# Performance work log

Measured on AMD Instinct MI355X. Metric: run time of the kernel, lower is better.

## Reference

```python
import jax, jax.numpy as jnp
import numpy as np

B, QL, DL = 256, 16, 512      # batch, query len, doc graph nodes
ND, NW, ED = 512, 50000, 300  # n_docs, vocab, embed dim
TOPK, K2, K4 = 40, 240, 192   # args.topk, ggnn2 keep, ggnn4 keep


def setup_inputs() -> dict:
    key = jax.random.key(0)
    ks = jax.random.split(key, 32)
    s = 0.1
    inp = {
        "emb": jax.random.normal(ks[0], (NW + 1, ED), jnp.float32),
        "qrl_token": jax.random.randint(ks[1], (B, QL), 0, NW),
        "doc_token": jax.random.randint(ks[2], (B, DL), 0, NW),
        "doc_ids": jax.random.randint(ks[3], (B,), 0, ND),
        "docs_adj": jax.random.uniform(ks[4], (ND, DL, DL), jnp.float32),
        "idf": jax.random.uniform(ks[5], (B, QL, 1), jnp.float32),
        "W_g1": jax.random.normal(ks[6], (6, QL, QL), jnp.float32) * s,
        "b_g1": jax.random.normal(ks[7], (6, QL), jnp.float32) * s,
        "w_g2": jax.random.normal(ks[8], (6,), jnp.float32) * s,
        "b_g2": jax.random.normal(ks[9], (6,), jnp.float32) * s,
        "W_g3": jax.random.normal(ks[10], (6, QL, QL), jnp.float32) * s,
        "b_g3": jax.random.normal(ks[11], (6, QL), jnp.float32) * s,
        "w_g4": jax.random.normal(ks[12], (6,), jnp.float32) * s,
        "b_g4": jax.random.normal(ks[13], (6,), jnp.float32) * s,
        "p1_w": jax.random.normal(ks[14], (QL,), jnp.float32) * s,
        "p1_b": jax.random.normal(ks[15], (1,), jnp.float32) * s,
        "p2_w": jax.random.normal(ks[16], (QL,), jnp.float32) * s,
        "p2_b": jax.random.normal(ks[17], (1,), jnp.float32) * s,
        "l1_w": jax.random.normal(ks[18], (64, 3 * TOPK), jnp.float32) * s,
        "l1_b": jax.random.normal(ks[19], (64,), jnp.float32) * s,
        "l2_w": jax.random.normal(ks[20], (32, 64), jnp.float32) * s,
        "l2_b": jax.random.normal(ks[21], (32,), jnp.float32) * s,
        "l3_w": jax.random.normal(ks[22], (1, 32), jnp.float32) * s,
        "l3_b": jax.random.normal(ks[23], (1,), jnp.float32) * s,
        "gated_w": jax.random.normal(ks[24], (1,), jnp.float32) * s,
        "gated_b": jax.random.normal(ks[25], (1,), jnp.float32) * s,
    }
    return inp


def _simmat(a_emb, b_emb):
    # cosine similarity [B, A, C]
    an = jnp.linalg.norm(a_emb, axis=2)[:, :, None] + 1e-9
    bn = jnp.linalg.norm(b_emb, axis=2)[:, None, :] + 1e-9
    return jnp.einsum("bad,bcd->bac", a_emb, b_emb) / (an * bn)


def _gate_mat(a, x, W, b):
    # GGNN gated update, W: [6, D, D] stacked (z0,z1,r0,r1,h0,h1)
    lin = lambda t, i: t @ W[i].T + b[i]
    z = jax.nn.sigmoid(lin(a, 0) + lin(x, 1))
    r = jax.nn.sigmoid(lin(a, 2) + lin(x, 3))
    h = jax.nn.relu(lin(a, 4) + lin(r * x, 5))
    return h * z + x * (1.0 - z)


def _gate_scalar(a, x, w, b):
    lin = lambda t, i: t * w[i] + b[i]
    z = jax.nn.sigmoid(lin(a, 0) + lin(x, 1))
    r = jax.nn.sigmoid(lin(a, 2) + lin(x, 3))
    h = jax.nn.relu(lin(a, 4) + lin(r * x, 5))
    return h * z + x * (1.0 - z)


def _sub_adj(A, idx):
    # A: [L, L], idx: [K] -> A[idx][:, idx]
    return A[idx][:, idx]


def reference(emb, qrl_token, doc_token, doc_ids, docs_adj, idf,
              W_g1, b_g1, w_g2, b_g2, W_g3, b_g3, w_g4, b_g4,
              p1_w, p1_b, p2_w, p2_b,
              l1_w, l1_b, l2_w, l2_b, l3_w, l3_b, gated_w, gated_b):
    qe = emb[qrl_token]               # [B, QL, ED]
    de = emb[doc_token]               # [B, DL, ED]
    feat = _simmat(qe, de).transpose(0, 2, 1)   # [B, DL, QL]
    topk0 = jax.lax.top_k(feat.transpose(0, 2, 1), TOPK)[0]  # [B, QL, TOPK]

    adj = docs_adj[doc_ids]           # [B, DL, DL]

    # ggnn1
    rep1 = _gate_mat(adj @ feat, feat, W_g1, b_g1)           # [B, DL, QL]

    # ggnn2 (scalar gates on projected feature + topk subgraph gather)
    x2 = rep1 @ p1_w[:, None] + p1_b                         # [B, DL, 1]
    feat_s = _gate_scalar(adj @ x2, x2, w_g2, b_g2)          # [B, DL, 1]
    score1, idx1 = jax.lax.top_k(feat_s[..., 0], K2)         # [B, K2]
    att_x1 = jnp.take_along_axis(rep1, idx1[:, :, None], axis=1)  # [B, K2, QL]
    adj_new = jax.vmap(_sub_adj)(adj, idx1)                  # [B, K2, K2]
    att_x1 = jnp.tanh(score1)[:, :, None] * att_x1

    # ggnn3
    rep3 = _gate_mat(adj_new @ att_x1, att_x1, W_g3, b_g3)   # [B, K2, QL]

    # ggnn4
    x4 = rep3 @ p2_w[:, None] + p2_b                         # [B, K2, 1]
    feat_s4 = _gate_scalar(adj_new @ x4, x4, w_g4, b_g4)
    score2, idx2 = jax.lax.top_k(feat_s4[..., 0], K4)        # [B, K4]
    att_x2 = jnp.take_along_axis(rep3, idx2[:, :, None], axis=1)  # [B, K4, QL]
    att_x2 = jnp.tanh(score2)[:, :, None] * att_x2

    att1 = jax.lax.top_k(att_x1.transpose(0, 2, 1), TOPK)[0]  # [B, QL, TOPK]
    att2 = jax.lax.top_k(att_x2.transpose(0, 2, 1), TOPK)[0]  # [B, QL, TOPK]
    att_x = jnp.concatenate([topk0, att1, att2], axis=-1)     # [B, QL, 3*TOPK]

    rel = jax.nn.relu(att_x @ l1_w.T + l1_b)
    rel = jax.nn.relu(rel @ l2_w.T + l2_b)
    rel = rel @ l3_w.T + l3_b                                 # [B, QL, 1]

    gated_weight = jax.nn.softmax(idf * gated_w + gated_b, axis=1)
    rel = rel * gated_weight
    scores = rel[..., 0].sum(-1, keepdims=True)               # [B, 1]
    return scores
```

## Files before the change

### kernel.cpp

```cpp
#include <hip/hip_runtime.h>
#include <math.h>

#define B_   256
#define QL_  16
#define DL_  512
#define ED_  300
#define K2_  240
#define K4_  192
#define NEGINF (-3.402823466e38f)

__device__ __forceinline__ float sigf(float x){ return 1.0f/(1.0f+__expf(-x)); }

__device__ __forceinline__ float dot16(const float (&a)[16], const float* w){
  float s = 0.f;
  #pragma unroll
  for (int i=0;i<4;i++){
    float4 ww = *(const float4*)(w + 4*i);
    s = fmaf(a[4*i+0], ww.x, s);
    s = fmaf(a[4*i+1], ww.y, s);
    s = fmaf(a[4*i+2], ww.z, s);
    s = fmaf(a[4*i+3], ww.w, s);
  }
  return s;
}

template<int N, int T>
__device__ void bitonic_desc(float* v, int* id){
  const int tid = threadIdx.x;
  for (int k = 2; k <= N; k <<= 1){
    for (int j = k >> 1; j > 0; j >>= 1){
      __syncthreads();
      for (int i = tid; i < N; i += T){
        const int l = i ^ j;
        if (l > i){
          const float vi = v[i], vl = v[l];
          const int ii = id[i], il = id[l];
          const bool before_l = (vl > vi) || (vl == vi && il < ii);
          const bool up = ((i & k) == 0);
          if (up == before_l){ v[i]=vl; v[l]=vi; id[i]=il; id[l]=ii; }
        }
      }
    }
  }
  __syncthreads();
}

template<int NREG>
__device__ __forceinline__ void wave_sort_desc(float (&v)[NREG], int lane){
  constexpr int TOT = NREG*64;
  #pragma unroll
  for (int k = 2; k <= TOT; k <<= 1){
    #pragma unroll
    for (int j = k>>1; j > 0; j >>= 1){
      if (j >= 64){
        const int jr = j >> 6;
        #pragma unroll
        for (int r = 0; r < NREG; r++){
          if ((r & jr) == 0){
            const int p = r | jr;
            const bool desc = (((r*64) & k) == 0);
            const float a = v[r], c = v[p];
            const float mx = fmaxf(a,c), mn = fminf(a,c);
            v[r] = desc ? mx : mn;
            v[p] = desc ? mn : mx;
          }
        }
      } else {
        #pragma unroll
        for (int r = 0; r < NREG; r++){
          const float ov = __shfl_xor(v[r], j);
          const bool desc = (((r*64 + lane) & k) == 0);
          const bool lower = (lane & j) == 0;
          v[r] = (lower == desc) ? fmaxf(v[r], ov) : fminf(v[r], ov);
        }
      }
    }
  }
}

__global__ __launch_bounds__(256) void k_feat(
    const float* __restrict__ emb, const int* __restrict__ qtok,
    const int* __restrict__ dtok,
    float* __restrict__ featdq, float* __restrict__ featqd)
{
  alignas(16) __shared__ float ql[16*304];
  __shared__ float qinv[16];
  __shared__ int toks[128];
  const int tid = threadIdx.x;
  const int b = blockIdx.x >> 2, d0 = (blockIdx.x & 3) * 128;
  #pragma unroll
  for (int q=0;q<16;q++){
    const int tokq = qtok[(size_t)b*QL_ + q];
    for (int e=tid; e<ED_; e+=256)
      ql[q*304+e] = emb[(size_t)tokq*ED_ + e];
  }
  if (tid < 128) toks[tid] = dtok[(size_t)b*DL_ + d0 + tid];
  __syncthreads();
  {
    const int q = tid >> 4, s = tid & 15;
    float ss = 0.f;
    for (int e=s;e<ED_;e+=16){ const float x = ql[q*304+e]; ss = fmaf(x,x,ss); }
    ss += __shfl_xor(ss,1); ss += __shfl_xor(ss,2);
    ss += __shfl_xor(ss,4); ss += __shfl_xor(ss,8);
    if (s == 0) qinv[q] = 1.f/(sqrtf(ss)+1e-9f);
  }
  __syncthreads();
  const int g = tid>>2, sub = tid&3;
  const float* e0p = emb + (size_t)toks[2*g+0]*ED_;
  const float* e1p = emb + (size_t)toks[2*g+1]*ED_;
  float acc[2][16];
  float ssr[2] = {0.f,0.f};
  #pragma unroll
  for (int r=0;r<2;r++)
    #pragma unroll
    for (int q=0;q<16;q++) acc[r][q] = 0.f;
  for (int i=0;i<19;i++){
    const int j = sub + 4*i;
    if (j < 75){
      const int e0 = 4*j;
      float4 d0v = *(const float4*)(e0p + e0);
      float4 d1v = *(const float4*)(e1p + e0);
      ssr[0] = fmaf(d0v.x,d0v.x, fmaf(d0v.y,d0v.y, fmaf(d0v.z,d0v.z, fmaf(d0v.w,d0v.w, ssr[0]))));
      ssr[1] = fmaf(d1v.x,d1v.x, fmaf(d1v.y,d1v.y, fmaf(d1v.z,d1v.z, fmaf(d1v.w,d1v.w, ssr[1]))));
      #pragma unroll
      for (int q=0;q<16;q++){
        float4 qv = *(const float4*)(&ql[q*304 + e0]);
        acc[0][q] = fmaf(d0v.x,qv.x, fmaf(d0v.y,qv.y, fmaf(d0v.z,qv.z, fmaf(d0v.w,qv.w, acc[0][q]))));
        acc[1][q] = fmaf(d1v.x,qv.x, fmaf(d1v.y,qv.y, fmaf(d1v.z,qv.z, fmaf(d1v.w,qv.w, acc[1][q]))));
      }
    }
  }
  #pragma unroll
  for (int r=0;r<2;r++){
    #pragma unroll
    for (int q=0;q<16;q++){
      float v = acc[r][q];
      v += __shfl_xor(v, 1);
      v += __shfl_xor(v, 2);
      acc[r][q] = v;
    }
    float sv = ssr[r];
    sv += __shfl_xor(sv, 1);
    sv += __shfl_xor(sv, 2);
    ssr[r] = sv;
  }
  const int r = sub & 1;
  const int d = d0 + 2*g + r;
  const float ssd = r ? ssr[1] : ssr[0];
  const float invd = 1.f/(sqrtf(ssd)+1e-9f);
  float vs[16];
  #pragma unroll
  for (int q=0;q<16;q++){
    const float v = r ? acc[1][q] : acc[0][q];
    vs[q] = v * invd * qinv[q];
  }
  if (sub < 2){
    float* fo = &featdq[((size_t)b*DL_ + d)*16];
    *(float4*)(fo+0)  = make_float4(vs[0],vs[1],vs[2],vs[3]);
    *(float4*)(fo+4)  = make_float4(vs[4],vs[5],vs[6],vs[7]);
    *(float4*)(fo+8)  = make_float4(vs[8],vs[9],vs[10],vs[11]);
    *(float4*)(fo+12) = make_float4(vs[12],vs[13],vs[14],vs[15]);
  } else {
    #pragma unroll
    for (int q=0;q<16;q++)
      featqd[((size_t)b*QL_+q)*DL_ + d] = vs[q];
  }
}

__global__ __launch_bounds__(256,3) void k_gemm512(
    const float* __restrict__ dadj, const int* __restrict__ doc_ids,
    const float* __restrict__ Bmat, const float* __restrict__ Wg,
    const float* __restrict__ bg, const float* __restrict__ pw,
    const float* __restrict__ pb, float* __restrict__ rep,
    float* __restrict__ xproj)
{
  __shared__ float fx[512*20];
  __shared__ float wl[1536];
  __shared__ float bl[96];
  __shared__ float pwl[16];
  const int tid = threadIdx.x;
  const int b = blockIdx.x >> 1, part = blockIdx.x & 1;
  const int m0 = part * 256;
  for (int idx = tid; idx < 512*16; idx += 256){
    fx[(idx>>4)*20 + (idx&15)] = Bmat[(size_t)b*512*16 + idx];
  }
  for (int idx = tid; idx < 1536; idx += 256) wl[idx] = Wg[idx];
  if (tid < 96) bl[tid] = bg[tid];
  if (tid < 16) pwl[tid] = pw[tid];
  __syncthreads();

  const int g = tid >> 2, sub = tid & 3;
  const int mb = m0 + 4*g;
  {
    const int lda = 512;
    const float* arow = dadj + (size_t)doc_ids[b] * 512 * 512;
    const float* r0 = arow + (size_t)mb * lda;
    constexpr int ITERS = 32;
    float acc[4][16];
    #pragma unroll
    for (int r=0;r<4;r++)
      #pragma unroll
      for (int q=0;q<16;q++) acc[r][q] = 0.f;
    int kk = sub*4;
    float4 c0 = *(const float4*)(r0 + kk);
    float4 c1 = *(const float4*)(r0 + lda + kk);
    float4 c2 = *(const float4*)(r0 + 2*lda + kk);
    float4 c3 = *(const float4*)(r0 + 3*lda + kk);
    for (int i = 0; i < ITERS; i++){
      const int kn = kk + ((i < ITERS-1) ? 16 : 0);
      float4 n0 = *(const float4*)(r0 + kn);
      float4 n1 = *(const float4*)(r0 + lda + kn);
      float4 n2 = *(const float4*)(r0 + 2*lda + kn);
      float4 n3 = *(const float4*)(r0 + 3*lda + kn);
      const float av[4][4] = {{c0.x,c0.y,c0.z,c0.w},{c1.x,c1.y,c1.z,c1.w},
                              {c2.x,c2.y,c2.z,c2.w},{c3.x,c3.y,c3.z,c3.w}};
      #pragma unroll
      for (int c = 0; c < 4; c++){
        const float* fr = &fx[(size_t)(kk + c)*20];
        float4 q0 = *(const float4*)(fr);
        float4 q1 = *(const float4*)(fr+4);
        float4 q2 = *(const float4*)(fr+8);
        float4 q3 = *(const float4*)(fr+12);
        const float qv[16] = {q0.x,q0.y,q0.z,q0.w, q1.x,q1.y,q1.z,q1.w,
                              q2.x,q2.y,q2.z,q2.w, q3.x,q3.y,q3.z,q3.w};
        #pragma unroll
        for (int r = 0; r < 4; r++){
          const float a_ = av[r][c];
          #pragma unroll
          for (int q = 0; q < 16; q++)
            acc[r][q] = fmaf(a_, qv[q], acc[r][q]);
        }
      }
      c0 = n0; c1 = n1; c2 = n2; c3 = n3;
      kk += 16;
    }
    #pragma unroll
    for (int r=0;r<4;r++)
      #pragma unroll
      for (int q=0;q<16;q++){
        float v = acc[r][q];
        v += __shfl_xor(v, 1);
        v += __shfl_xor(v, 2);
        acc[r][q] = v;
      }
    const int m = mb + sub;
    float a[16], x[16];
    #pragma unroll
    for (int q=0;q<16;q++)
      a[q] = (sub==0)?acc[0][q]:(sub==1)?acc[1][q]:(sub==2)?acc[2][q]:acc[3][q];
    {
      const float* xr = &fx[(size_t)m*20];
      float4 x0 = *(const float4*)(xr),   x1 = *(const float4*)(xr+4);
      float4 x2v = *(const float4*)(xr+8), x3 = *(const float4*)(xr+12);
      x[0]=x0.x; x[1]=x0.y; x[2]=x0.z; x[3]=x0.w;
      x[4]=x1.x; x[5]=x1.y; x[6]=x1.z; x[7]=x1.w;
      x[8]=x2v.x; x[9]=x2v.y; x[10]=x2v.z; x[11]=x2v.w;
      x[12]=x3.x; x[13]=x3.y; x[14]=x3.z; x[15]=x3.w;
    }
    float z[16], rr[16];
    #pragma unroll
    for (int q=0;q<16;q++){
      const float s0 = bl[q] + bl[16+q]
                     + dot16(a, &wl[q*16]) + dot16(x, &wl[256 + q*16]);
      z[q] = sigf(s0);
      const float s1 = bl[32+q] + bl[48+q]
                     + dot16(a, &wl[512 + q*16]) + dot16(x, &wl[768 + q*16]);
      rr[q] = sigf(s1);
    }
    float rx[16];
    #pragma unroll
    for (int q=0;q<16;q++) rx[q] = rr[q]*x[q];
    float out[16]; float xp = 0.f;
    #pragma unroll
    for (int q=0;q<16;q++){
      const float s = bl[64+q] + bl[80+q]
                    + dot16(a, &wl[1024 + q*16]) + dot16(rx, &wl[1280 + q*16]);
      const float h = fmaxf(s, 0.f);
      const float o = h*z[q] + x[q]*(1.f - z[q]);
      out[q] = o;
      xp = fmaf(o, pwl[q], xp);
    }
    float* rp = &rep[((size_t)b*512 + m)*16];
    *(float4*)(rp+0)  = make_float4(out[0],out[1],out[2],out[3]);
    *(float4*)(rp+4)  = make_float4(out[4],out[5],out[6],out[7]);
    *(float4*)(rp+8)  = make_float4(out[8],out[9],out[10],out[11]);
    *(float4*)(rp+12) = make_float4(out[12],out[13],out[14],out[15]);
    xproj[(size_t)b*512 + m] = xp + pb[0];
  }
}

__global__ __launch_bounds__(1024) void k_chain(
    const float* __restrict__ dadj, const int* __restrict__ dids,
    const float* __restrict__ featqd, const float* __restrict__ rep1,
    const float* __restrict__ x2g,
    const float* __restrict__ wg2, const float* __restrict__ bg2,
    const float* __restrict__ Wg3, const float* __restrict__ bg3,
    const float* __restrict__ wg4, const float* __restrict__ bg4,
    const float* __restrict__ p2w, const float* __restrict__ p2b,
    const float* __restrict__ l1w, const float* __restrict__ l1b,
    const float* __restrict__ l2w, const float* __restrict__ l2b,
    const float* __restrict__ l3w, const float* __restrict__ l3b,
    const float* __restrict__ idf, const float* __restrict__ gw,
    const float* __restrict__ gb,
    float* __restrict__ adjnew, float* __restrict__ outp)
{
  extern __shared__ float sm[];
  float* fx   = sm;
  float* repl = fx + 4800;
  float* w1l  = repl + 4800;
  float* w2l  = w1l + 7936;
  float* wl   = w2l + 2176;
  float* attl = wl + 1536;
  float* rel1 = attl + 1920;
  float* rel2 = rel1 + 1024;
  float* xv   = rel2 + 512;
  float* sval = xv + 512;
  int*   sidx = (int*)(sval + 512);
  int*   il   = sidx + 512;
  float* bl   = (float*)(il + 240);
  float* pwl  = bl + 96;

  const int tid = threadIdx.x, b = blockIdx.x;
  const int wave = tid >> 6, lane = tid & 63;
  const float* abase = dadj + (size_t)dids[b]*512*512;

  if (tid < 512) xv[tid] = x2g[(size_t)b*512 + tid];
  __syncthreads();

  if (wave < 8){
    const int g = tid >> 2, sub = tid & 3;
    const float w0=wg2[0],w1=wg2[1],w2=wg2[2],w3=wg2[3],w4=wg2[4],w5=wg2[5];
    const float c0=bg2[0],c1=bg2[1],c2=bg2[2],c3=bg2[3],c4=bg2[4],c5=bg2[5];
    for (int p = 0; p < 4; p++){
      const int m = p*128 + g;
      const float* row = abase + (size_t)m*512;
      float s = 0.f;
      #pragma unroll 4
      for (int i=0;i<32;i++){
        const int kk = i*16 + sub*4;
        float4 a4 = *(const float4*)(row + kk);
        float4 xq = *(const float4*)(&xv[kk]);
        s = fmaf(a4.x,xq.x,s); s = fmaf(a4.y,xq.y,s);
        s = fmaf(a4.z,xq.z,s); s = fmaf(a4.w,xq.w,s);
      }
      s += __shfl_xor(s,1); s += __shfl_xor(s,2);
      if (sub == 0){
        const float x = xv[m];
        const float z = sigf(fmaf(s,w0,c0) + fmaf(x,w1,c1));
        const float r = sigf(fmaf(s,w2,c2) + fmaf(x,w3,c3));
        const float h = fmaxf(fmaf(s,w4,c4) + fmaf(r*x,w5,c5), 0.f);
        sval[m] = h*z + x*(1.f - z);
        sidx[m] = m;
      }
    }
  } else {
    const int w8 = wave - 8;
    #pragma unroll
    for (int t=0;t<2;t++){
      const int q = w8*2 + t;
      const float* src = featqd + ((size_t)b*QL_ + q)*512;
      float v[8];
      #pragma unroll
      for (int r=0;r<8;r++) v[r] = src[lane + 64*r];
      wave_sort_desc<8>(v, lane);
      if (lane < 40) attl[q*120 + lane] = v[0];
    }
    for (int idx = tid-512; idx < 7680; idx += 512){
      const int u = idx/120, k2 = idx - u*120;
      w1l[u*124 + k2] = l1w[idx];
    }
    for (int idx = tid-512; idx < 2048; idx += 512)
      w2l[(idx>>6)*68 + (idx&63)] = l2w[idx];
  }
  bitonic_desc<512,1024>(sval, sidx);

  if (tid < K2_){
    const int rowi = sidx[tid];
    il[tid] = rowi;
    const float tv = tanhf(sval[tid]);
    const float* rr = rep1 + ((size_t)b*512 + rowi)*16;
    float4 r0 = *(const float4*)(rr),   r1 = *(const float4*)(rr+4);
    float4 r2 = *(const float4*)(rr+8), r3 = *(const float4*)(rr+12);
    float* o = &fx[(size_t)tid*20];
    *(float4*)(o+0)  = make_float4(tv*r0.x,tv*r0.y,tv*r0.z,tv*r0.w);
    *(float4*)(o+4)  = make_float4(tv*r1.x,tv*r1.y,tv*r1.z,tv*r1.w);
    *(float4*)(o+8)  = make_float4(tv*r2.x,tv*r2.y,tv*r2.z,tv*r2.w);
    *(float4*)(o+12) = make_float4(tv*r3.x,tv*r3.y,tv*r3.z,tv*r3.w);
  }
  __syncthreads();

  for (int idx = tid; idx < 1536; idx += 1024) wl[idx] = Wg3[idx];
  if (tid < 96) bl[tid] = bg3[tid];
  if (tid < 16) pwl[tid] = p2w[tid];
  {
    const int rt = wave, jt = lane;
    int jc[4];
    #pragma unroll
    for (int c=0;c<4;c++){
      const int j = jt + 64*c;
      jc[c] = (j < K2_) ? il[j] : 0;
    }
    for (int p=0;p<15;p++){
      const int r = rt + p*16;
      const float* row = abase + (size_t)il[r]*512;
      float* orow = adjnew + ((size_t)b*K2_ + r)*K2_;
      #pragma unroll
      for (int c=0;c<4;c++){
        const int j = jt + 64*c;
        if (j < K2_) orow[j] = row[jc[c]];
      }
    }
  }
  __syncthreads();

  {
    const int q = wave;
    float v[4];
    #pragma unroll
    for (int r=0;r<4;r++){
      const int idx = lane + 64*r;
      v[r] = (idx < K2_) ? fx[(size_t)idx*20 + q] : NEGINF;
    }
    wave_sort_desc<4>(v, lane);
    if (lane < 40) attl[q*120 + 40 + lane] = v[0];
  }

  {
    const int g = tid >> 2, sub = tid & 3;
    if (g < K2_){
      const int m = g;
      const float* r0 = adjnew + ((size_t)b*K2_ + m)*K2_;
      float acc[16];
      #pragma unroll
      for (int q=0;q<16;q++) acc[q] = 0.f;
      for (int i=0;i<15;i++){
        const int kk = i*16 + sub*4;
        float4 a4 = *(const float4*)(r0 + kk);
        const float av[4] = {a4.x, a4.y, a4.z, a4.w};
        #pragma unroll
        for (int c=0;c<4;c++){
          const float* fr = &fx[(size_t)(kk + c)*20];
          float4 q0 = *(const float4*)(fr);
          float4 q1 = *(const float4*)(fr+4);
          float4 q2 = *(const float4*)(fr+8);
          float4 q3 = *(const float4*)(fr+12);
          const float qv[16] = {q0.x,q0.y,q0.z,q0.w, q1.x,q1.y,q1.z,q1.w,
                                q2.x,q2.y,q2.z,q2.w, q3.x,q3.y,q3.z,q3.w};
          #pragma unroll
          for (int q=0;q<16;q++)
            acc[q] = fmaf(av[c], qv[q], acc[q]);
        }
      }
      #pragma unroll
      for (int q=0;q<16;q++){
        float v = acc[q];
        v += __shfl_xor(v, 1);
        v += __shfl_xor(v, 2);
        acc[q] = v;
      }
      float x[16];
      {
        const float* xr = &fx[(size_t)m*20];
        float4 x0 = *(const float4*)(xr),   x1 = *(const float4*)(xr+4);
        float4 x2v = *(const float4*)(xr+8), x3 = *(const float4*)(xr+12);
        x[0]=x0.x; x[1]=x0.y; x[2]=x0.z; x[3]=x0.w;
        x[4]=x1.x; x[5]=x1.y; x[6]=x1.z; x[7]=x1.w;
        x[8]=x2v.x; x[9]=x2v.y; x[10]=x2v.z; x[11]=x2v.w;
        x[12]=x3.x; x[13]=x3.y; x[14]=x3.z; x[15]=x3.w;
      }
      float rx[16];
      #pragma unroll
      for (int q=0;q<16;q++){
        const float s1 = bl[32+q] + bl[48+q]
                       + dot16(acc, &wl[512 + q*16]) + dot16(x, &wl[768 + q*16]);
        rx[q] = sigf(s1) * x[q];
      }
      float xp = 0.f;
      #pragma unroll
      for (int j=0;j<4;j++){
        const int q = sub*4 + j;
        const float s0 = bl[q] + bl[16+q]
                       + dot16(acc, &wl[q*16]) + dot16(x, &wl[256 + q*16]);
        const float z = sigf(s0);
        const float s = bl[64+q] + bl[80+q]
                      + dot16(acc, &wl[1024 + q*16]) + dot16(rx, &wl[1280 + q*16]);
        const float h = fmaxf(s, 0.f);
        const float o = h*z + x[q]*(1.f - z);
        repl[(size_t)m*20 + q] = o;
        xp = fmaf(o, pwl[q], xp);
      }
      xp += __shfl_xor(xp,1); xp += __shfl_xor(xp,2);
      if (sub == 0) xv[m] = xp + p2b[0];
    }
  }
  __syncthreads();

  {
    const int g = tid >> 2, sub = tid & 3;
    const float w0=wg4[0],w1=wg4[1],w2=wg4[2],w3=wg4[3],w4=wg4[4],w5=wg4[5];
    const float c0=bg4[0],c1=bg4[1],c2=bg4[2],c3=bg4[3],c4=bg4[4],c5=bg4[5];
    if (g < K2_){
      const float* row = adjnew + ((size_t)b*K2_ + g)*K2_;
      float s = 0.f;
      #pragma unroll
      for (int i=0;i<15;i++){
        const int kk = i*16 + sub*4;
        float4 a4 = *(const float4*)(row + kk);
        float4 xq = *(const float4*)(&xv[kk]);
        s = fmaf(a4.x,xq.x,s); s = fmaf(a4.y,xq.y,s);
        s = fmaf(a4.z,xq.z,s); s = fmaf(a4.w,xq.w,s);
      }
      s += __shfl_xor(s,1); s += __shfl_xor(s,2);
      if (sub == 0){
        const float x = xv[g];
        const float z = sigf(fmaf(s,w0,c0) + fmaf(x,w1,c1));
        const float r = sigf(fmaf(s,w2,c2) + fmaf(x,w3,c3));
        const float h = fmaxf(fmaf(s,w4,c4) + fmaf(r*x,w5,c5), 0.f);
        sval[g] = h*z + x*(1.f - z);
        sidx[g] = g;
      }
    }
    if (tid >= 960 && tid < 976){
      sval[K2_ + tid - 960] = NEGINF;
      sidx[K2_ + tid - 960] = 0x7fffffff;
    }
  }
  bitonic_desc<256,1024>(sval, sidx);

  if (tid < K4_){
    const int rowi = sidx[tid];
    const float tv = tanhf(sval[tid]);
    const float* rr = &repl[(size_t)rowi*20];
    float4 r0 = *(const float4*)(rr),   r1 = *(const float4*)(rr+4);
    float4 r2 = *(const float4*)(rr+8), r3 = *(const float4*)(rr+12);
    float* o = &fx[(size_t)tid*20];
    *(float4*)(o+0)  = make_float4(tv*r0.x,tv*r0.y,tv*r0.z,tv*r0.w);
    *(float4*)(o+4)  = make_float4(tv*r1.x,tv*r1.y,tv*r1.z,tv*r1.w);
    *(float4*)(o+8)  = make_float4(tv*r2.x,tv*r2.y,tv*r2.z,tv*r2.w);
    *(float4*)(o+12) = make_float4(tv*r3.x,tv*r3.y,tv*r3.z,tv*r3.w);
  }
  __syncthreads();

  {
    const int q = wave;
    float v[4];
    #pragma unroll
    for (int r=0;r<4;r++){
      const int idx = lane + 64*r;
      v[r] = (idx < K4_) ? fx[(size_t)idx*20 + q] : NEGINF;
    }
    wave_sort_desc<4>(v, lane);
    if (lane < 40) attl[q*120 + 80 + lane] = v[0];
  }
  __syncthreads();

  {
    const int q = tid >> 6, u = tid & 63;
    float acc = l1b[u];
    #pragma unroll
    for (int k4=0;k4<30;k4++){
      float4 av = *(const float4*)(&attl[q*120 + k4*4]);
      float4 wv = *(const float4*)(&w1l[u*124 + k4*4]);
      acc = fmaf(av.x,wv.x,acc); acc = fmaf(av.y,wv.y,acc);
      acc = fmaf(av.z,wv.z,acc); acc = fmaf(av.w,wv.w,acc);
    }
    rel1[q*64 + u] = fmaxf(acc, 0.f);
  }
  __syncthreads();
  if (tid < 512){
    const int q = tid >> 5, u = tid & 31;
    float acc = l2b[u];
    #pragma unroll
    for (int k4=0;k4<16;k4++){
      float4 av = *(const float4*)(&rel1[q*64 + k4*4]);
      float4 wv = *(const float4*)(&w2l[u*68 + k4*4]);
      acc = fmaf(av.x,wv.x,acc); acc = fmaf(av.y,wv.y,acc);
      acc = fmaf(av.z,wv.z,acc); acc = fmaf(av.w,wv.w,acc);
    }
    rel2[q*32 + u] = fmaxf(acc, 0.f);
  }
  __syncthreads();
  if (tid < 16){
    float acc = l3b[0];
    #pragma unroll
    for (int k=0;k<32;k++) acc = fmaf(rel2[tid*32+k], l3w[k], acc);
    const float gv = fmaf(idf[(size_t)b*16 + tid], gw[0], gb[0]);
    float mx = gv;
    mx = fmaxf(mx, __shfl_xor(mx, 1));
    mx = fmaxf(mx, __shfl_xor(mx, 2));
    mx = fmaxf(mx, __shfl_xor(mx, 4));
    mx = fmaxf(mx, __shfl_xor(mx, 8));
    const float e = __expf(gv - mx);
    float se = e;
    se += __shfl_xor(se, 1); se += __shfl_xor(se, 2);
    se += __shfl_xor(se, 4); se += __shfl_xor(se, 8);
    float val = acc * (e / se);
    val += __shfl_xor(val, 1); val += __shfl_xor(val, 2);
    val += __shfl_xor(val, 4); val += __shfl_xor(val, 8);
    if (tid == 0) outp[b] = val;
  }
}

extern "C" void kernel_launch(void* const* d_in, const int* in_sizes, int n_in,
                              void* d_out, int out_size, void* d_ws, size_t ws_size,
                              hipStream_t stream)
{
  const float* emb  = (const float*)d_in[0];
  const int*   qtok = (const int*)d_in[1];
  const int*   dtok = (const int*)d_in[2];
  const int*   dids = (const int*)d_in[3];
  const float* dadj = (const float*)d_in[4];
  const float* idf  = (const float*)d_in[5];
  const float* Wg1  = (const float*)d_in[6];
  const float* bg1  = (const float*)d_in[7];
  const float* wg2  = (const float*)d_in[8];
  const float* bg2  = (const float*)d_in[9];
  const float* Wg3  = (const float*)d_in[10];
  const float* bg3  = (const float*)d_in[11];
  const float* wg4  = (const float*)d_in[12];
  const float* bg4  = (const float*)d_in[13];
  const float* p1w  = (const float*)d_in[14];
  const float* p1b  = (const float*)d_in[15];
  const float* p2w  = (const float*)d_in[16];
  const float* p2b  = (const float*)d_in[17];
  const float* l1w  = (const float*)d_in[18];
  const float* l1b  = (const float*)d_in[19];
  const float* l2w  = (const float*)d_in[20];
  const float* l2b  = (const float*)d_in[21];
  const float* l3w  = (const float*)d_in[22];
  const float* l3b  = (const float*)d_in[23];
  const float* gw   = (const float*)d_in[24];
  const float* gb   = (const float*)d_in[25];
  float* out = (float*)d_out;

  float* ws = (float*)d_ws;
  size_t off = 0;
  auto alloc = [&](size_t n)->float*{ float* p = ws + off; off += (n + 3) & ~(size_t)3; return p; };
  float* featdq = alloc((size_t)B_*DL_*QL_);
  float* featqd = alloc((size_t)B_*DL_*QL_);
  float* rep1   = alloc((size_t)B_*DL_*QL_);
  float* x2     = alloc((size_t)B_*DL_);
  float* adjnew = alloc((size_t)B_*K2_*K2_);

  const size_t chain_lds = 26592u * 4u;

  k_feat<<<B_*4, 256, 0, stream>>>(emb, qtok, dtok, featdq, featqd);
  k_gemm512<<<B_*2, 256, 0, stream>>>(
      dadj, dids, featdq, Wg1, bg1, p1w, p1b, rep1, x2);
  k_chain<<<B_, 1024, chain_lds, stream>>>(
      dadj, dids, featqd, rep1, x2, wg2, bg2, Wg3, bg3, wg4, bg4,
      p2w, p2b, l1w, l1b, l2w, l2b, l3w, l3b, idf, gw, gb,
      adjnew, out);
}
```

Before: 259.1 us.

## Split ggnn2 adjacency matvec into separate wide kernel and rebalance chain phases

Moves the 512x512 adjacency-times-vector plus scalar gate out of the one-block-per-batch chain kernel into a new kernel that uses four 256-thread blocks per batch, writing gate scores to a workspace buffer. This gives more parallelism and memory-level concurrency for the largest adjacency read. The chain kernel now spreads its work differently across waves: weight staging overlaps the gather, the top-k for the first attention runs alongside the adjacency sub-gather, and one barrier is removed. The cost is an extra launch and a global round trip for the scores.

```diff
diff --git a/kernel.cpp b/kernel.cpp
--- a/kernel.cpp
+++ b/kernel.cpp
@@ -289,11 +289,60 @@
   }
 }
 
-__global__ __launch_bounds__(1024) void k_chain(
+__global__ __launch_bounds__(256) void k_s1(
+    const float* __restrict__ dadj, const int* __restrict__ dids,
+    const float* __restrict__ x2g, const float* __restrict__ wsc,
+    const float* __restrict__ bsc, float* __restrict__ svalg)
+{
+  alignas(16) __shared__ float xv[512];
+  const int tid = threadIdx.x;
+  const int b = blockIdx.x >> 2, part = blockIdx.x & 3;
+  for (int i = tid; i < 512; i += 256) xv[i] = x2g[(size_t)b*512 + i];
+  __syncthreads();
+  const float* abase = dadj + (size_t)dids[b]*512*512;
+  const int g = tid>>2, sub = tid&3;
+  const float w0=wsc[0],w1=wsc[1],w2=wsc[2],w3=wsc[3],w4=wsc[4],w5=wsc[5];
+  const float c0=bsc[0],c1=bsc[1],c2=bsc[2],c3=bsc[3],c4=bsc[4],c5=bsc[5];
+  #pragma unroll
+  for (int pp=0; pp<2; pp++){
+    const int m = part*128 + pp*64 + g;
+    const float* row = abase + (size_t)m*512;
+    float s = 0.f;
+    #pragma unroll
+    for (int ii=0; ii<8; ii++){
+      const int k0 = ii*64 + sub*4;
+      float4 a0 = *(const float4*)(row + k0);
+      float4 a1 = *(const float4*)(row + k0 + 16);
+      float4 a2 = *(const float4*)(row + k0 + 32);
+      float4 a3 = *(const float4*)(row + k0 + 48);
+      float4 x0 = *(const float4*)(&xv[k0]);
+      float4 x1 = *(const float4*)(&xv[k0+16]);
+      float4 x2v = *(const float4*)(&xv[k0+32]);
+      float4 x3 = *(const float4*)(&xv[k0+48]);
+      s = fmaf(a0.x,x0.x,s); s = fmaf(a0.y,x0.y,s);
+      s = fmaf(a0.z,x0.z,s); s = fmaf(a0.w,x0.w,s);
+      s = fmaf(a1.x,x1.x,s); s = fmaf(a1.y,x1.y,s);
+      s = fmaf(a1.z,x1.z,s); s = fmaf(a1.w,x1.w,s);
+      s = fmaf(a2.x,x2v.x,s); s = fmaf(a2.y,x2v.y,s);
+      s = fmaf(a2.z,x2v.z,s); s = fmaf(a2.w,x2v.w,s);
+      s = fmaf(a3.x,x3.x,s); s = fmaf(a3.y,x3.y,s);
+      s = fmaf(a3.z,x3.z,s); s = fmaf(a3.w,x3.w,s);
+    }
+    s += __shfl_xor(s,1); s += __shfl_xor(s,2);
+    if (sub == 0){
+      const float x = xv[m];
+      const float z = sigf(fmaf(s,w0,c0) + fmaf(x,w1,c1));
+      const float r = sigf(fmaf(s,w2,c2) + fmaf(x,w3,c3));
+      const float h = fmaxf(fmaf(s,w4,c4) + fmaf(r*x,w5,c5), 0.f);
+      svalg[(size_t)b*512 + m] = h*z + x*(1.f - z);
+    }
+  }
+}
+
+__global__ __launch_bounds__(1024) void k_chain2(
     const float* __restrict__ dadj, const int* __restrict__ dids,
     const float* __restrict__ featqd, const float* __restrict__ rep1,
-    const float* __restrict__ x2g,
-    const float* __restrict__ wg2, const float* __restrict__ bg2,
+    const float* __restrict__ svalg,
     const float* __restrict__ Wg3, const float* __restrict__ bg3,
     const float* __restrict__ wg4, const float* __restrict__ bg4,
     const float* __restrict__ p2w, const float* __restrict__ p2b,
@@ -324,53 +373,15 @@
   const int wave = tid >> 6, lane = tid & 63;
   const float* abase = dadj + (size_t)dids[b]*512*512;
 
-  if (tid < 512) xv[tid] = x2g[(size_t)b*512 + tid];
-  __syncthreads();
-
-  if (wave < 8){
-    const int g = tid >> 2, sub = tid & 3;
-    const float w0=wg2[0],w1=wg2[1],w2=wg2[2],w3=wg2[3],w4=wg2[4],w5=wg2[5];
-    const float c0=bg2[0],c1=bg2[1],c2=bg2[2],c3=bg2[3],c4=bg2[4],c5=bg2[5];
-    for (int p = 0; p < 4; p++){
-      const int m = p*128 + g;
-      const float* row = abase + (size_t)m*512;
-      float s = 0.f;
-      #pragma unroll 4
-      for (int i=0;i<32;i++){
-        const int kk = i*16 + sub*4;
-        float4 a4 = *(const float4*)(row + kk);
-        float4 xq = *(const float4*)(&xv[kk]);
-        s = fmaf(a4.x,xq.x,s); s = fmaf(a4.y,xq.y,s);
-        s = fmaf(a4.z,xq.z,s); s = fmaf(a4.w,xq.w,s);
-      }
-      s += __shfl_xor(s,1); s += __shfl_xor(s,2);
-      if (sub == 0){
-        const float x = xv[m];
-        const float z = sigf(fmaf(s,w0,c0) + fmaf(x,w1,c1));
-        const float r = sigf(fmaf(s,w2,c2) + fmaf(x,w3,c3));
-        const float h = fmaxf(fmaf(s,w4,c4) + fmaf(r*x,w5,c5), 0.f);
-        sval[m] = h*z + x*(1.f - z);
-        sidx[m] = m;
-      }
-    }
-  } else {
-    const int w8 = wave - 8;
-    #pragma unroll
-    for (int t=0;t<2;t++){
-      const int q = w8*2 + t;
-      const float* src = featqd + ((size_t)b*QL_ + q)*512;
-      float v[8];
-      #pragma unroll
-      for (int r=0;r<8;r++) v[r] = src[lane + 64*r];
-      wave_sort_desc<8>(v, lane);
-      if (lane < 40) attl[q*120 + lane] = v[0];
-    }
-    for (int idx = tid-512; idx < 7680; idx += 512){
-      const int u = idx/120, k2 = idx - u*120;
-      w1l[u*124 + k2] = l1w[idx];
-    }
-    for (int idx = tid-512; idx < 2048; idx += 512)
-      w2l[(idx>>6)*68 + (idx&63)] = l2w[idx];
+  if (tid < 512){ sval[tid] = svalg[(size_t)b*512 + tid]; sidx[tid] = tid; }
+  {
+    const int q = wave;
+    const float* src = featqd + ((size_t)b*QL_ + q)*512;
+    float v[8];
+    #pragma unroll
+    for (int r=0;r<8;r++) v[r] = src[lane + 64*r];
+    wave_sort_desc<8>(v, lane);
+    if (lane < 40) attl[q*120 + lane] = v[0];
   }
   bitonic_desc<512,1024>(sval, sidx);
 
@@ -386,44 +397,53 @@
     *(float4*)(o+4)  = make_float4(tv*r1.x,tv*r1.y,tv*r1.z,tv*r1.w);
     *(float4*)(o+8)  = make_float4(tv*r2.x,tv*r2.y,tv*r2.z,tv*r2.w);
     *(float4*)(o+12) = make_float4(tv*r3.x,tv*r3.y,tv*r3.z,tv*r3.w);
-  }
-  __syncthreads();
-
-  for (int idx = tid; idx < 1536; idx += 1024) wl[idx] = Wg3[idx];
-  if (tid < 96) bl[tid] = bg3[tid];
-  if (tid < 16) pwl[tid] = p2w[tid];
-  {
-    const int rt = wave, jt = lane;
+  } else {
+    for (int idx = tid-240; idx < 7680; idx += 784){
+      const int u = idx/120, k2 = idx - u*120;
+      w1l[u*124 + k2] = l1w[idx];
+    }
+    for (int idx = tid-240; idx < 2048; idx += 784)
+      w2l[(idx>>6)*68 + (idx&63)] = l2w[idx];
+  }
+  __syncthreads();
+
+  if (wave < 12){
     int jc[4];
     #pragma unroll
     for (int c=0;c<4;c++){
-      const int j = jt + 64*c;
+      const int j = lane + 64*c;
       jc[c] = (j < K2_) ? il[j] : 0;
     }
-    for (int p=0;p<15;p++){
-      const int r = rt + p*16;
+    #pragma unroll
+    for (int p=0;p<20;p++){
+      const int r = wave*20 + p;
       const float* row = abase + (size_t)il[r]*512;
       float* orow = adjnew + ((size_t)b*K2_ + r)*K2_;
       #pragma unroll
       for (int c=0;c<4;c++){
-        const int j = jt + 64*c;
+        const int j = lane + 64*c;
         if (j < K2_) orow[j] = row[jc[c]];
       }
     }
-  }
-  __syncthreads();
-
-  {
-    const int q = wave;
-    float v[4];
-    #pragma unroll
-    for (int r=0;r<4;r++){
-      const int idx = lane + 64*r;
-      v[r] = (idx < K2_) ? fx[(size_t)idx*20 + q] : NEGINF;
-    }
-    wave_sort_desc<4>(v, lane);
-    if (lane < 40) attl[q*120 + 40 + lane] = v[0];
-  }
+  } else {
+    const int t4 = tid - 768;
+    for (int idx = t4; idx < 1536; idx += 256) wl[idx] = Wg3[idx];
+    if (t4 < 96) bl[t4] = bg3[t4];
+    if (t4 < 16) pwl[t4] = p2w[t4];
+    #pragma unroll
+    for (int t=0;t<4;t++){
+      const int q = (wave-12)*4 + t;
+      float v[4];
+      #pragma unroll
+      for (int r=0;r<4;r++){
+        const int idx = lane + 64*r;
+        v[r] = (idx < K2_) ? fx[(size_t)idx*20 + q] : NEGINF;
+      }
+      wave_sort_desc<4>(v, lane);
+      if (lane < 40) attl[q*120 + 40 + lane] = v[0];
+    }
+  }
+  __syncthreads();
 
   {
     const int g = tid >> 2, sub = tid & 3;
@@ -640,6 +660,7 @@
   float* featqd = alloc((size_t)B_*DL_*QL_);
   float* rep1   = alloc((size_t)B_*DL_*QL_);
   float* x2     = alloc((size_t)B_*DL_);
+  float* svalg  = alloc((size_t)B_*DL_);
   float* adjnew = alloc((size_t)B_*K2_*K2_);
 
   const size_t chain_lds = 26592u * 4u;
@@ -647,8 +668,9 @@
   k_feat<<<B_*4, 256, 0, stream>>>(emb, qtok, dtok, featdq, featqd);
   k_gemm512<<<B_*2, 256, 0, stream>>>(
       dadj, dids, featdq, Wg1, bg1, p1w, p1b, rep1, x2);
-  k_chain<<<B_, 1024, chain_lds, stream>>>(
-      dadj, dids, featqd, rep1, x2, wg2, bg2, Wg3, bg3, wg4, bg4,
+  k_s1<<<B_*4, 256, 0, stream>>>(dadj, dids, x2, wg2, bg2, svalg);
+  k_chain2<<<B_, 1024, chain_lds, stream>>>(
+      dadj, dids, featqd, rep1, svalg, Wg3, bg3, wg4, bg4,
       p2w, p2b, l1w, l1b, l2w, l2b, l3w, l3b, idf, gw, gb,
       adjnew, out);
 }
```

Result: slower. 276.5 us (+6.7%).
